# Kernel optimization log

Hardware: AMD Instinct MI355X
Metric: run time of the kernel (lower is better)

Reference implementation:

```python
import jax, jax.numpy as jnp
import numpy as np


def setup_inputs() -> dict:
    key = jax.random.key(0)
    k1, k2, k3, k4, k5, k6 = jax.random.split(key, 6)
    NODE, TAG, E, D, B = 100000, 10000, 4, 32, 524288
    INIT = 0.001
    return {
        "tag_table": INIT * jax.random.normal(k1, (TAG, D), dtype=jnp.float32),
        "node_tables": INIT * jax.random.normal(k2, (E, NODE, D), dtype=jnp.float32),
        "activate": jnp.zeros((NODE, E), dtype=jnp.float32),
        "pos_node": jax.random.randint(k3, (B,), 0, NODE),
        "pos_tag": jax.random.randint(k4, (B,), 0, TAG),
        "neg_node": jax.random.randint(k5, (B,), 0, NODE),
        "neg_tag": jax.random.randint(k6, (B,), 0, TAG),
    }


def _node_tag_dist(node_tables, tag_table, node_list, tag_list):
    # tag_emb: [B, D]; per-table node emb: [E, B, D]
    tag_emb = tag_table[tag_list]
    node_emb = node_tables[:, node_list, :]  # [E, B, D]
    # eu_dist = -sum(x*y, dim=1) for each table -> [B, E]
    dists = -jnp.einsum("ebd,bd->be", node_emb, tag_emb)
    min_idx = jnp.argmin(dists, axis=1)          # [B]
    dist = jnp.min(dists, axis=1, keepdims=True)  # [B, 1]
    return dist, min_idx


def reference(tag_table, node_tables, activate, pos_node, pos_tag, neg_node, neg_tag):
    # positive branch (pos=True): update activate counter with argmin choices
    pos_dist, pos_idx = _node_tag_dist(node_tables, tag_table, pos_node, pos_tag)
    activate_new = activate.at[pos_node, pos_idx].add(1.0)
    pos_loss = -jnp.sum(jax.nn.log_sigmoid(-pos_dist))
    # negative branch (no counter update)
    neg_dist, _ = _node_tag_dist(node_tables, tag_table, neg_node, neg_tag)
    neg_loss = -jnp.sum(jax.nn.log_sigmoid(neg_dist))
    loss = pos_loss + neg_loss
    return loss, activate_new
```

## Files before the change

kernel.cpp:

```cpp
#include <hip/hip_runtime.h>

#define NODES 100000
#define NTAG  10000
#define NE    4
#define ND    32
#define NB    524288

constexpr int TPB   = 256;
constexpr int BNODE = 32;
constexpr int NBUCK = NODES / BNODE;
constexpr int CAP   = 512;
constexpr int MBLK  = 1024;

constexpr int STPB  = 1024;
constexpr int CHUNK = 8192;
constexpr int SBLK  = 2 * NB / CHUNK;

constexpr size_t OFF_REC = 16384;
constexpr size_t WS_NEED = OFF_REC + (size_t)NBUCK * CAP * 4;

template <int CTRL>
__device__ __forceinline__ double bfly_dpp(double v) {
    const int lo = __builtin_amdgcn_update_dpp(0, __double2loint(v), CTRL, 0xF, 0xF, true);
    const int hi = __builtin_amdgcn_update_dpp(0, __double2hiint(v), CTRL, 0xF, 0xF, true);
    return __hiloint2double(hi, lo);
}
__device__ __forceinline__ double bfly_swz4(double v) {
    const int lo = __builtin_amdgcn_ds_swizzle(__double2loint(v), 0x101F);
    const int hi = __builtin_amdgcn_ds_swizzle(__double2hiint(v), 0x101F);
    return __hiloint2double(hi, lo);
}
template <int CTRL>
__device__ __forceinline__ float bflyf_dpp(float v) {
    return __int_as_float(__builtin_amdgcn_update_dpp(0, __float_as_int(v), CTRL, 0xF, 0xF, true));
}
__device__ __forceinline__ float bflyf_swz4(float v) {
    return __int_as_float(__builtin_amdgcn_ds_swizzle(__float_as_int(v), 0x101F));
}


__global__ __launch_bounds__(TPB) void init_kernel(float* __restrict__ out,
                                                   int* __restrict__ cnt) {
    const int i = blockIdx.x * TPB + threadIdx.x;
    if (i < NBUCK)  cnt[i] = 0;
    if (i == NBUCK) out[0] = 0.f;
}

__global__ __launch_bounds__(STPB) void scatter_kernel(
    const int* __restrict__ pos_node, const int* __restrict__ pos_tag,
    const int* __restrict__ neg_node, const int* __restrict__ neg_tag,
    int* __restrict__ cnt_g, uint32_t* __restrict__ rec)
{
    __shared__ uint32_t lrec[CHUNK];
    __shared__ int lcnt[NBUCK];
    __shared__ int lbase[NBUCK];

    const int tid = threadIdx.x;
    const int blk = blockIdx.x;
    const bool is_pos = blk < (SBLK / 2);
    const int  base = (is_pos ? blk : blk - SBLK / 2) * CHUNK;
    const int* __restrict__ nsrc = is_pos ? pos_node : neg_node;
    const int* __restrict__ tsrc = is_pos ? pos_tag  : neg_tag;

    for (int i = tid; i < NBUCK; i += STPB) lcnt[i] = 0;
    __syncthreads();

    #pragma unroll
    for (int r = 0; r < CHUNK / STPB; ++r) {
        const int i = r * STPB + tid;
        const int node = nsrc[base + i];
        const int tag  = tsrc[base + i];
        lrec[i] = ((uint32_t)node << 15) | ((uint32_t)tag << 1) | (is_pos ? 1u : 0u);
        atomicAdd(&lcnt[node >> 5], 1);
    }
    __syncthreads();

    for (int i = tid; i < NBUCK; i += STPB) {
        const int c = lcnt[i];
        lbase[i] = c ? atomicAdd(&cnt_g[i], c) : 0;
        lcnt[i]  = 0;
    }
    __syncthreads();

    #pragma unroll
    for (int r = 0; r < CHUNK / STPB; ++r) {
        const int i = r * STPB + tid;
        const uint32_t v = lrec[i];
        const int bk = (int)(v >> 20);
        const int p  = lbase[bk] + atomicAdd(&lcnt[bk], 1);
        if (p < CAP)
            rec[(size_t)bk * CAP + p] = v;
    }
}

__global__ __launch_bounds__(TPB, 4) void main_kernel(
    const float* __restrict__ tag_table, const float* __restrict__ node_tables,
    const float* __restrict__ act,
    const int* __restrict__ cnt_g, const uint32_t* __restrict__ rec,
    float* __restrict__ out)
{
    __shared__ float    nlds[2][NE * BNODE * ND];
    __shared__ uint32_t recs_s[2][CAP];
    __shared__ uint32_t hist[BNODE * NE];
    __shared__ float sm[TPB / 64];

    const int tid = threadIdx.x;
    const int g   = tid & 7;
    const int grp = tid >> 3;
    const uint32_t goff = (uint32_t)g << 4;

    const char* tagb = (const char*)tag_table;
    const float4* __restrict__ nsrc4 = (const float4*)node_tables;

    int bks[4]; int nb = 0;
    #pragma unroll
    for (int k = 0; k < 4; ++k) {
        const int b = blockIdx.x + k * MBLK;
        if (b < NBUCK) bks[nb++] = b;
    }

    if (tid < BNODE * NE) hist[tid] = 0;

    int n_cur = min(cnt_g[bks[0]], CAP);
    {
        const uint32_t nbase0 = (uint32_t)bks[0] * BNODE;
        float4 st[4];
        #pragma unroll
        for (int r = 0; r < 4; ++r) {
            const int f = r * TPB + tid;
            st[r] = nsrc4[(size_t)(f >> 8) * (NODES * 8) + (size_t)nbase0 * 8 + (f & 255)];
        }
        uint32_t rc0 = 0, rc1 = 0;
        const uint32_t* __restrict__ rg = rec + (size_t)bks[0] * CAP;
        if (tid < n_cur)       rc0 = rg[tid];
        if (tid + 256 < n_cur) rc1 = rg[tid + 256];
        #pragma unroll
        for (int r = 0; r < 4; ++r) ((float4*)nlds[0])[r * TPB + tid] = st[r];
        if (tid < n_cur)       recs_s[0][tid] = rc0;
        if (tid + 256 < n_cur) recs_s[0][tid + 256] = rc1;
    }
    __syncthreads();

    float local = 0.f;
    int cur = 0;

    for (int ib = 0; ib < nb; ++ib) {
        const int bk = bks[ib];
        const int n  = n_cur;
        const uint32_t nbase = (uint32_t)bk * BNODE;

        const bool have_nxt = (ib + 1 < nb);
        float4 st[4];
        uint32_t rc0 = 0, rc1 = 0;
        int n_nxt = 0;
        if (have_nxt) {
            const int bkn = bks[ib + 1];
            n_nxt = min(cnt_g[bkn], CAP);
            const uint32_t nbasen = (uint32_t)bkn * BNODE;
            #pragma unroll
            for (int r = 0; r < 4; ++r) {
                const int f = r * TPB + tid;
                st[r] = nsrc4[(size_t)(f >> 8) * (NODES * 8) + (size_t)nbasen * 8 + (f & 255)];
            }
            const uint32_t* __restrict__ rg = rec + (size_t)bks[ib + 1] * CAP;
            if (tid < n_nxt)       rc0 = rg[tid];
            if (tid + 256 < n_nxt) rc1 = rg[tid + 256];
        }

        const float*    bufc = nlds[cur];
        const uint32_t* recc = recs_s[cur];
        for (int j = grp; j < n; j += 32) {
            const uint32_t rr = recc[j];
            const uint32_t node = rr >> 15, tag = (rr >> 1) & 0x3FFFu;
            const int lr = (int)(node & 31u);

            const float4 cc = *(const float4*)(tagb + ((tag << 7) + goff));
            const float* rp = bufc + (lr << 5) + (g << 2);
            const float4 a0 = *(const float4*)(rp);
            const float4 a1 = *(const float4*)(rp + 1024);
            const float4 a2 = *(const float4*)(rp + 2048);
            const float4 a3 = *(const float4*)(rp + 3072);

            float q0 = fmaf(a0.w, cc.w, fmaf(a0.z, cc.z, fmaf(a0.y, cc.y, a0.x * cc.x)));
            float q1 = fmaf(a1.w, cc.w, fmaf(a1.z, cc.z, fmaf(a1.y, cc.y, a1.x * cc.x)));
            float q2 = fmaf(a2.w, cc.w, fmaf(a2.z, cc.z, fmaf(a2.y, cc.y, a2.x * cc.x)));
            float q3 = fmaf(a3.w, cc.w, fmaf(a3.z, cc.z, fmaf(a3.y, cc.y, a3.x * cc.x)));

            q0 += bflyf_dpp<0xB1>(q0); q1 += bflyf_dpp<0xB1>(q1);
            q2 += bflyf_dpp<0xB1>(q2); q3 += bflyf_dpp<0xB1>(q3);
            q0 += bflyf_dpp<0x4E>(q0); q1 += bflyf_dpp<0x4E>(q1);
            q2 += bflyf_dpp<0x4E>(q2); q3 += bflyf_dpp<0x4E>(q3);
            q0 += bflyf_swz4(q0); q1 += bflyf_swz4(q1);
            q2 += bflyf_swz4(q2); q3 += bflyf_swz4(q3);

            float m1 = q0; int idx = 0;
            if (q1 > m1) { m1 = q1; idx = 1; }
            if (q2 > m1) { m1 = q2; idx = 2; }
            if (q3 > m1) { m1 = q3; idx = 3; }
            const float h01 = fmaxf(q0, q1), l01 = fminf(q0, q1);
            const float h23 = fmaxf(q2, q3), l23 = fminf(q2, q3);
            const float m2 = fmaxf(fminf(h01, h23), (h01 > h23) ? l01 : l23);

            float best = m1;
            if (m1 - m2 < 1e-7f) {
                const double tx = (double)cc.x, ty = (double)cc.y, tz = (double)cc.z, tw = (double)cc.w;
                double d0 = (double)a0.x*tx + (double)a0.y*ty + (double)a0.z*tz + (double)a0.w*tw;
                double d1 = (double)a1.x*tx + (double)a1.y*ty + (double)a1.z*tz + (double)a1.w*tw;
                double d2 = (double)a2.x*tx + (double)a2.y*ty + (double)a2.z*tz + (double)a2.w*tw;
                double d3 = (double)a3.x*tx + (double)a3.y*ty + (double)a3.z*tz + (double)a3.w*tw;
                d0 += bfly_dpp<0xB1>(d0); d1 += bfly_dpp<0xB1>(d1);
                d2 += bfly_dpp<0xB1>(d2); d3 += bfly_dpp<0xB1>(d3);
                d0 += bfly_dpp<0x4E>(d0); d1 += bfly_dpp<0x4E>(d1);
                d2 += bfly_dpp<0x4E>(d2); d3 += bfly_dpp<0x4E>(d3);
                d0 += bfly_swz4(d0); d1 += bfly_swz4(d1);
                d2 += bfly_swz4(d2); d3 += bfly_swz4(d3);
                double b = d0; idx = 0;
                if (d1 > b) { b = d1; idx = 1; }
                if (d2 > b) { b = d2; idx = 2; }
                if (d3 > b) { b = d3; idx = 3; }
                best = (float)b;
            }

            const bool  pos = (rr & 1u);
            const float x   = pos ? -best : best;
            const float e   = __expf(-fabsf(x));
            local += fmaxf(x, 0.f) + __logf(1.f + e);

            if (pos && g == 0)
                atomicAdd(&hist[(node & 31u) * NE + idx], 1u);
        }

        __syncthreads();

        if (tid < BNODE * NE) {
            const uint32_t cell = nbase * NE + tid;
            out[1 + cell] = act[cell] + (float)hist[tid];
            hist[tid] = 0;
        }

        if (have_nxt) {
            const int nxt = cur ^ 1;
            #pragma unroll
            for (int r = 0; r < 4; ++r) ((float4*)nlds[nxt])[r * TPB + tid] = st[r];
            if (tid < n_nxt)       recs_s[nxt][tid] = rc0;
            if (tid + 256 < n_nxt) recs_s[nxt][tid + 256] = rc1;
            __syncthreads();
            cur = nxt;
            n_cur = n_nxt;
        }
    }

    #pragma unroll
    for (int off = 1; off < 64; off <<= 1) local += __shfl_xor(local, off, 64);
    if ((tid & 63) == 0) sm[tid >> 6] = local;
    __syncthreads();
    if (tid == 0) {
        float tot = 0.f;
        #pragma unroll
        for (int w = 0; w < TPB / 64; ++w) tot += sm[w];
        atomicAdd(out, tot * 0.125f);
    }
}


__global__ __launch_bounds__(TPB) void fb_init(const float* __restrict__ act,
                                               float* __restrict__ out,
                                               double* __restrict__ ws, int npart) {
    int i = blockIdx.x * TPB + threadIdx.x;
    if (i < NODES * NE) out[1 + i] = act[i];
    if (i < npart)      ws[i] = 0.0;
}

__global__ __launch_bounds__(TPB) void fb_main(
    const float* __restrict__ tag_table, const float* __restrict__ node_tables,
    const int* __restrict__ pos_node, const int* __restrict__ pos_tag,
    const int* __restrict__ neg_node, const int* __restrict__ neg_tag,
    float* __restrict__ out, double* __restrict__ ws, int npart)
{
    const int tid = threadIdx.x;
    const int g   = tid & 7;
    const int grp = tid >> 3;
    const uint32_t goff = (uint32_t)g << 4;
    const int total = 2 * NB;
    constexpr int FNB = 2048, FGRP = FNB * (TPB / 8);

    const char* tagb  = (const char*)tag_table;
    const char* nodb0 = (const char*)node_tables;
    const char* nodb1 = nodb0 + (size_t)NODES * 128;
    const char* nodb2 = nodb1 + (size_t)NODES * 128;
    const char* nodb3 = nodb2 + (size_t)NODES * 128;

    float local = 0.f;
    for (int s = blockIdx.x * (TPB / 8) + grp; s < total; s += FGRP) {
        const bool is_pos = s < NB;
        const int  b    = is_pos ? s : s - NB;
        const int  node = is_pos ? pos_node[b] : neg_node[b];
        const int  tag  = is_pos ? pos_tag[b]  : neg_tag[b];
        const uint32_t no = ((uint32_t)node << 7) + goff, to = ((uint32_t)tag << 7) + goff;
        const float4 t  = *(const float4*)(tagb  + to);
        const float4 n0 = *(const float4*)(nodb0 + no);
        const float4 n1 = *(const float4*)(nodb1 + no);
        const float4 n2 = *(const float4*)(nodb2 + no);
        const float4 n3 = *(const float4*)(nodb3 + no);
        const double tx = (double)t.x, ty = (double)t.y, tz = (double)t.z, tw = (double)t.w;
        double q0 = (double)n0.x*tx + (double)n0.y*ty + (double)n0.z*tz + (double)n0.w*tw;
        double q1 = (double)n1.x*tx + (double)n1.y*ty + (double)n1.z*tz + (double)n1.w*tw;
        double q2 = (double)n2.x*tx + (double)n2.y*ty + (double)n2.z*tz + (double)n2.w*tw;
        double q3 = (double)n3.x*tx + (double)n3.y*ty + (double)n3.z*tz + (double)n3.w*tw;
        #pragma unroll
        for (int off = 1; off < 8; off <<= 1) {
            q0 += __shfl_xor(q0, off, 64); q1 += __shfl_xor(q1, off, 64);
            q2 += __shfl_xor(q2, off, 64); q3 += __shfl_xor(q3, off, 64);
        }
        double best = q0; int idx = 0;
        if (q1 > best) { best = q1; idx = 1; }
        if (q2 > best) { best = q2; idx = 2; }
        if (q3 > best) { best = q3; idx = 3; }
        const float x = is_pos ? (float)(-best) : (float)best;
        const float e = __expf(-fabsf(x));
        local += fmaxf(x, 0.f) + __logf(1.f + e);
        if (is_pos && g == 0) atomicAdd(out + 1 + ((size_t)node << 2) + idx, 1.0f);
    }
    #pragma unroll
    for (int off = 1; off < 64; off <<= 1) local += __shfl_xor(local, off, 64);
    __shared__ double sm[TPB / 64];
    if ((tid & 63) == 0) sm[tid >> 6] = (double)local;
    __syncthreads();
    if (tid == 0) {
        double tot = 0.0;
        #pragma unroll
        for (int w = 0; w < TPB / 64; ++w) tot += sm[w];
        atomicAdd(&ws[blockIdx.x & (npart - 1)], tot * 0.125);
    }
}

__global__ __launch_bounds__(TPB) void fb_final(const double* __restrict__ loss_part,
                                                float* __restrict__ out, int npart) {
    __shared__ double sm[TPB];
    double v = 0.0;
    for (int i = threadIdx.x; i < npart; i += TPB) v += loss_part[i];
    sm[threadIdx.x] = v;
    __syncthreads();
    for (int s = TPB / 2; s > 0; s >>= 1) {
        if (threadIdx.x < s) sm[threadIdx.x] += sm[threadIdx.x + s];
        __syncthreads();
    }
    if (threadIdx.x == 0) out[0] = (float)sm[0];
}


extern "C" void kernel_launch(void* const* d_in, const int* in_sizes, int n_in,
                              void* d_out, int out_size, void* d_ws, size_t ws_size,
                              hipStream_t stream) {
    const float* tag_table   = (const float*)d_in[0];
    const float* node_tables = (const float*)d_in[1];
    const float* activate    = (const float*)d_in[2];
    const int*   pos_node    = (const int*)d_in[3];
    const int*   pos_tag     = (const int*)d_in[4];
    const int*   neg_node    = (const int*)d_in[5];
    const int*   neg_tag     = (const int*)d_in[6];
    float* out = (float*)d_out;

    if (ws_size >= WS_NEED) {
        int*      cnt = (int*)d_ws;
        uint32_t* rec = (uint32_t*)((char*)d_ws + OFF_REC);

        hipLaunchKernelGGL(init_kernel, dim3((NBUCK + TPB) / TPB + 1), dim3(TPB), 0, stream,
                           out, cnt);
        hipLaunchKernelGGL(scatter_kernel, dim3(SBLK), dim3(STPB), 0, stream,
                           pos_node, pos_tag, neg_node, neg_tag, cnt, rec);
        hipLaunchKernelGGL(main_kernel, dim3(MBLK), dim3(TPB), 0, stream,
                           tag_table, node_tables, activate, cnt, rec, out);
    } else {
        double* ws = (double*)d_ws;
        int npart = 1;
        while (npart * 2 <= 2048 && (size_t)(npart * 2) * sizeof(double) <= ws_size) npart *= 2;
        const int init_blocks = (NODES * NE + TPB - 1) / TPB;
        hipLaunchKernelGGL(fb_init, dim3(init_blocks), dim3(TPB), 0, stream,
                           activate, out, ws, npart);
        hipLaunchKernelGGL(fb_main, dim3(2048), dim3(TPB), 0, stream,
                           tag_table, node_tables, pos_node, pos_tag, neg_node, neg_tag,
                           out, ws, npart);
        hipLaunchKernelGGL(fb_final, dim3(1), dim3(TPB), 0, stream, ws, out, npart);
    }
}
```

Before: 67.49 us.

## Stage node tiles and records via direct global-to-LDS loads with 512-thread blocks

```diff
diff --git a/kernel.cpp b/kernel.cpp
--- a/kernel.cpp
+++ b/kernel.cpp
@@ -6,7 +6,7 @@
 #define ND    32
 #define NB    524288
 
-constexpr int TPB   = 256;
+constexpr int TPB   = 512;
 constexpr int BNODE = 32;
 constexpr int NBUCK = NODES / BNODE;
 constexpr int CAP   = 512;
@@ -18,6 +18,17 @@
 
 constexpr size_t OFF_REC = 16384;
 constexpr size_t WS_NEED = OFF_REC + (size_t)NBUCK * CAP * 4;
+
+__device__ __forceinline__ void gload_lds16(const void* g, void* l) {
+    __builtin_amdgcn_global_load_lds(
+        (const __attribute__((address_space(1))) unsigned int*)g,
+        (__attribute__((address_space(3))) unsigned int*)l, 16, 0, 0);
+}
+__device__ __forceinline__ void gload_lds4(const void* g, void* l) {
+    __builtin_amdgcn_global_load_lds(
+        (const __attribute__((address_space(1))) unsigned int*)g,
+        (__attribute__((address_space(3))) unsigned int*)l, 4, 0, 0);
+}
 
 template <int CTRL>
 __device__ __forceinline__ double bfly_dpp(double v) {
@@ -39,9 +50,9 @@
 }
 
 
-__global__ __launch_bounds__(TPB) void init_kernel(float* __restrict__ out,
+__global__ __launch_bounds__(256) void init_kernel(float* __restrict__ out,
                                                    int* __restrict__ cnt) {
-    const int i = blockIdx.x * TPB + threadIdx.x;
+    const int i = blockIdx.x * 256 + threadIdx.x;
     if (i < NBUCK)  cnt[i] = 0;
     if (i == NBUCK) out[0] = 0.f;
 }
@@ -93,7 +104,7 @@
     }
 }
 
-__global__ __launch_bounds__(TPB, 4) void main_kernel(
+__global__ __launch_bounds__(TPB, 8) void main_kernel(
     const float* __restrict__ tag_table, const float* __restrict__ node_tables,
     const float* __restrict__ act,
     const int* __restrict__ cnt_g, const uint32_t* __restrict__ rec,
@@ -104,72 +115,56 @@
     __shared__ uint32_t hist[BNODE * NE];
     __shared__ float sm[TPB / 64];
 
-    const int tid = threadIdx.x;
-    const int g   = tid & 7;
-    const int grp = tid >> 3;
+    const int tid  = threadIdx.x;
+    const int g    = tid & 7;
+    const int grp  = tid >> 3;
+    const int wave = tid >> 6;
     const uint32_t goff = (uint32_t)g << 4;
 
     const char* tagb = (const char*)tag_table;
     const float4* __restrict__ nsrc4 = (const float4*)node_tables;
 
-    int bks[4]; int nb = 0;
-    #pragma unroll
-    for (int k = 0; k < 4; ++k) {
-        const int b = blockIdx.x + k * MBLK;
-        if (b < NBUCK) bks[nb++] = b;
-    }
+    const int nb = 1 + (NBUCK - 1 - blockIdx.x) / MBLK;
+
+    auto stage = [&](int b, int bk) {
+        const uint32_t nbase = (uint32_t)bk * BNODE;
+        #pragma unroll
+        for (int r = 0; r < 2; ++r) {
+            const int f = r * TPB + tid;
+            const float4* gs = &nsrc4[(size_t)(f >> 8) * (NODES * 8)
+                                      + (size_t)nbase * 8 + (f & 255)];
+            char* ld = (char*)nlds[b] + (size_t)(r * TPB + wave * 64) * 16;
+            gload_lds16(gs, ld);
+        }
+        const uint32_t* rg = rec + (size_t)bk * CAP;
+        char* ld = (char*)recs_s[b] + (size_t)wave * 256;
+        gload_lds4(rg + tid, ld);
+    };
 
     if (tid < BNODE * NE) hist[tid] = 0;
 
-    int n_cur = min(cnt_g[bks[0]], CAP);
-    {
-        const uint32_t nbase0 = (uint32_t)bks[0] * BNODE;
-        float4 st[4];
-        #pragma unroll
-        for (int r = 0; r < 4; ++r) {
-            const int f = r * TPB + tid;
-            st[r] = nsrc4[(size_t)(f >> 8) * (NODES * 8) + (size_t)nbase0 * 8 + (f & 255)];
-        }
-        uint32_t rc0 = 0, rc1 = 0;
-        const uint32_t* __restrict__ rg = rec + (size_t)bks[0] * CAP;
-        if (tid < n_cur)       rc0 = rg[tid];
-        if (tid + 256 < n_cur) rc1 = rg[tid + 256];
-        #pragma unroll
-        for (int r = 0; r < 4; ++r) ((float4*)nlds[0])[r * TPB + tid] = st[r];
-        if (tid < n_cur)       recs_s[0][tid] = rc0;
-        if (tid + 256 < n_cur) recs_s[0][tid + 256] = rc1;
-    }
+    int n_cur = min(cnt_g[blockIdx.x], CAP);
+    stage(0, blockIdx.x);
     __syncthreads();
 
     float local = 0.f;
     int cur = 0;
 
     for (int ib = 0; ib < nb; ++ib) {
-        const int bk = bks[ib];
+        const int bk = blockIdx.x + ib * MBLK;
         const int n  = n_cur;
         const uint32_t nbase = (uint32_t)bk * BNODE;
 
         const bool have_nxt = (ib + 1 < nb);
-        float4 st[4];
-        uint32_t rc0 = 0, rc1 = 0;
-        int n_nxt = 0;
         if (have_nxt) {
-            const int bkn = bks[ib + 1];
-            n_nxt = min(cnt_g[bkn], CAP);
-            const uint32_t nbasen = (uint32_t)bkn * BNODE;
-            #pragma unroll
-            for (int r = 0; r < 4; ++r) {
-                const int f = r * TPB + tid;
-                st[r] = nsrc4[(size_t)(f >> 8) * (NODES * 8) + (size_t)nbasen * 8 + (f & 255)];
-            }
-            const uint32_t* __restrict__ rg = rec + (size_t)bks[ib + 1] * CAP;
-            if (tid < n_nxt)       rc0 = rg[tid];
-            if (tid + 256 < n_nxt) rc1 = rg[tid + 256];
+            const int bkn = bk + MBLK;
+            stage(cur ^ 1, bkn);
+            n_cur = min(cnt_g[bkn], CAP);
         }
 
         const float*    bufc = nlds[cur];
         const uint32_t* recc = recs_s[cur];
-        for (int j = grp; j < n; j += 32) {
+        for (int j = grp; j < n; j += TPB / 8) {
             const uint32_t rr = recc[j];
             const uint32_t node = rr >> 15, tag = (rr >> 1) & 0x3FFFu;
             const int lr = (int)(node & 31u);
@@ -237,17 +232,8 @@
             out[1 + cell] = act[cell] + (float)hist[tid];
             hist[tid] = 0;
         }
-
-        if (have_nxt) {
-            const int nxt = cur ^ 1;
-            #pragma unroll
-            for (int r = 0; r < 4; ++r) ((float4*)nlds[nxt])[r * TPB + tid] = st[r];
-            if (tid < n_nxt)       recs_s[nxt][tid] = rc0;
-            if (tid + 256 < n_nxt) recs_s[nxt][tid + 256] = rc1;
-            __syncthreads();
-            cur = nxt;
-            n_cur = n_nxt;
-        }
+        __syncthreads();
+        cur ^= 1;
     }
 
     #pragma unroll
@@ -263,15 +249,15 @@
 }
 
 
-__global__ __launch_bounds__(TPB) void fb_init(const float* __restrict__ act,
+__global__ __launch_bounds__(256) void fb_init(const float* __restrict__ act,
                                                float* __restrict__ out,
                                                double* __restrict__ ws, int npart) {
-    int i = blockIdx.x * TPB + threadIdx.x;
+    int i = blockIdx.x * 256 + threadIdx.x;
     if (i < NODES * NE) out[1 + i] = act[i];
     if (i < npart)      ws[i] = 0.0;
 }
 
-__global__ __launch_bounds__(TPB) void fb_main(
+__global__ __launch_bounds__(256) void fb_main(
     const float* __restrict__ tag_table, const float* __restrict__ node_tables,
     const int* __restrict__ pos_node, const int* __restrict__ pos_tag,
     const int* __restrict__ neg_node, const int* __restrict__ neg_tag,
@@ -282,7 +268,7 @@
     const int grp = tid >> 3;
     const uint32_t goff = (uint32_t)g << 4;
     const int total = 2 * NB;
-    constexpr int FNB = 2048, FGRP = FNB * (TPB / 8);
+    constexpr int FNB = 2048, FGRP = FNB * 32;
 
     const char* tagb  = (const char*)tag_table;
     const char* nodb0 = (const char*)node_tables;
@@ -291,7 +277,7 @@
     const char* nodb3 = nodb2 + (size_t)NODES * 128;
 
     float local = 0.f;
-    for (int s = blockIdx.x * (TPB / 8) + grp; s < total; s += FGRP) {
+    for (int s = blockIdx.x * 32 + grp; s < total; s += FGRP) {
         const bool is_pos = s < NB;
         const int  b    = is_pos ? s : s - NB;
         const int  node = is_pos ? pos_node[b] : neg_node[b];
@@ -323,25 +309,25 @@
     }
     #pragma unroll
     for (int off = 1; off < 64; off <<= 1) local += __shfl_xor(local, off, 64);
-    __shared__ double sm[TPB / 64];
+    __shared__ double sm[4];
     if ((tid & 63) == 0) sm[tid >> 6] = (double)local;
     __syncthreads();
     if (tid == 0) {
         double tot = 0.0;
         #pragma unroll
-        for (int w = 0; w < TPB / 64; ++w) tot += sm[w];
+        for (int w = 0; w < 4; ++w) tot += sm[w];
         atomicAdd(&ws[blockIdx.x & (npart - 1)], tot * 0.125);
     }
 }
 
-__global__ __launch_bounds__(TPB) void fb_final(const double* __restrict__ loss_part,
+__global__ __launch_bounds__(256) void fb_final(const double* __restrict__ loss_part,
                                                 float* __restrict__ out, int npart) {
-    __shared__ double sm[TPB];
+    __shared__ double sm[256];
     double v = 0.0;
-    for (int i = threadIdx.x; i < npart; i += TPB) v += loss_part[i];
+    for (int i = threadIdx.x; i < npart; i += 256) v += loss_part[i];
     sm[threadIdx.x] = v;
     __syncthreads();
-    for (int s = TPB / 2; s > 0; s >>= 1) {
+    for (int s = 128; s > 0; s >>= 1) {
         if (threadIdx.x < s) sm[threadIdx.x] += sm[threadIdx.x + s];
         __syncthreads();
     }
@@ -365,7 +351,7 @@
         int*      cnt = (int*)d_ws;
         uint32_t* rec = (uint32_t*)((char*)d_ws + OFF_REC);
 
-        hipLaunchKernelGGL(init_kernel, dim3((NBUCK + TPB) / TPB + 1), dim3(TPB), 0, stream,
+        hipLaunchKernelGGL(init_kernel, dim3((NBUCK + 256) / 256 + 1), dim3(256), 0, stream,
                            out, cnt);
         hipLaunchKernelGGL(scatter_kernel, dim3(SBLK), dim3(STPB), 0, stream,
                            pos_node, pos_tag, neg_node, neg_tag, cnt, rec);
@@ -375,12 +361,12 @@
         double* ws = (double*)d_ws;
         int npart = 1;
         while (npart * 2 <= 2048 && (size_t)(npart * 2) * sizeof(double) <= ws_size) npart *= 2;
-        const int init_blocks = (NODES * NE + TPB - 1) / TPB;
-        hipLaunchKernelGGL(fb_init, dim3(init_blocks), dim3(TPB), 0, stream,
+        const int init_blocks = (NODES * NE + 255) / 256;
+        hipLaunchKernelGGL(fb_init, dim3(init_blocks), dim3(256), 0, stream,
                            activate, out, ws, npart);
-        hipLaunchKernelGGL(fb_main, dim3(2048), dim3(TPB), 0, stream,
+        hipLaunchKernelGGL(fb_main, dim3(2048), dim3(256), 0, stream,
                            tag_table, node_tables, pos_node, pos_tag, neg_node, neg_tag,
                            out, ws, npart);
-        hipLaunchKernelGGL(fb_final, dim3(1), dim3(TPB), 0, stream, ws, out, npart);
-    }
-}
+        hipLaunchKernelGGL(fb_final, dim3(1), dim3(256), 0, stream, ws, out, npart);
+    }
+}
```

Result: faster. 57.54 us (-14.7%).
